# Optimization experiments

Hardware: AMD Instinct MI355X
Metric: run time of the kernel (lower is better)

Reference implementation:

```python
import jax, jax.numpy as jnp
import numpy as np

V, D, B, L = 8000, 256, 64, 64
CONCENTRATION = 5.0  # config['model']['args']['concentrator_factor']
GAW = 0.5            # initial value of _lambda parameter
EPS_COS = 1e-8       # torch cosine_similarity eps


def setup_inputs() -> dict:
    key = jax.random.key(0)
    ks = jax.random.split(key, 8)
    concepts_list = jax.random.randint(ks[0], (B, L), 0, V)
    concepts_length = jax.random.randint(ks[1], (B,), 0, L)
    contrastive_mask = jax.random.randint(ks[2], (B, V), 0, 2).astype(jnp.int32)
    # raw edge matrix, then row-range normalization as in init_params
    edge_raw = jax.random.uniform(ks[3], (V, V), dtype=jnp.float32)
    rng = (edge_raw.max(axis=1) - edge_raw.min(axis=1))[:, None]
    edge_matrix = edge_raw / (rng + (rng == 0).astype(jnp.float32))
    affectiveness = jax.random.uniform(ks[4], (V,), dtype=jnp.float32)
    embed_w = jax.random.normal(ks[5], (V, D), dtype=jnp.float32)
    embed_kb_w = jax.random.normal(ks[6], (V, D), dtype=jnp.float32)
    lam = jnp.full((V,), GAW, dtype=jnp.float32)
    return {
        "concepts_list": concepts_list,
        "concepts_length": concepts_length,
        "contrastive_mask": contrastive_mask,
        "edge_matrix": edge_matrix,
        "affectiveness": affectiveness,
        "embed_w": embed_w,
        "embed_kb_w": embed_kb_w,
        "lam": lam,
    }


def reference(concepts_list, concepts_length, contrastive_mask,
              edge_matrix, affectiveness, embed_w, embed_kb_w, lam):
    # [B, L, D] concept token embeddings
    concepts_embedded = embed_w[concepts_list]
    # valid-prefix mask per row: positions < concepts_length[i]
    pos_mask = (jnp.arange(L)[None, :] < concepts_length[:, None])  # [B, L] bool
    denom = jnp.maximum(concepts_length, 1).astype(concepts_embedded.dtype)[:, None]
    # per-row masked mean (rows with length 0 -> zeros, matching empty_tensor)
    row_mean = (concepts_embedded * pos_mask[..., None]).sum(axis=1) / denom  # [B, D]
    context_representation = row_mean.mean(axis=0)  # [D]
    # |cosine similarity| between context and every KB embedding -> [V]
    ctx_norm = jnp.linalg.norm(context_representation)
    kb_norms = jnp.linalg.norm(embed_kb_w, axis=1)
    cosine_similarity = jnp.abs(
        (embed_kb_w @ context_representation) / jnp.maximum(kb_norms * ctx_norm, EPS_COS)
    )
    # [B, L, V] local graph rows for each concept token
    local_graph = edge_matrix[concepts_list]
    rel = local_graph * cosine_similarity          # broadcast over V
    aff = (local_graph > 0).astype(local_graph.dtype) * affectiveness
    concepts_weights = lam * rel + (1.0 - lam) * aff  # [B, L, V]
    concepts_weights = jnp.where(contrastive_mask[:, None, :] == 0, 1e-9, concepts_weights)
    attn = jax.nn.softmax(concepts_weights * CONCENTRATION, axis=2)  # [B, L, V]
    concepts_embedding = jnp.einsum('blv,vd->bld', attn, embed_kb_w)  # [B, L, D]
    # masked mean over valid prefix (length 0 -> zeros)
    concepts_embedding = (concepts_embedding * pos_mask[..., None]).sum(axis=1) / denom  # [B, D]
    local_nodes = jnp.broadcast_to(embed_kb_w[None], (B, V, D))
    return concepts_embedding, local_nodes
```

## Files before the change

kernel.cpp:

```cpp
#include <hip/hip_runtime.h>
#include <cstddef>
#include <cstdint>
#include <cmath>

#define V 8000
#define D 256
#define B 64
#define L 64
#define SPLIT 8
#define NCH 100
#define VC 80
#define BT 16

#define PART_OFF 0
#define CTX_OFF  16384
#define W1_OFF   16640
#define W0_OFF   24640
#define A_OFF    32640
#define P_OFF    544640

typedef float f32x4 __attribute__((ext_vector_type(4)));

__global__ void k1_ctx(const int* __restrict__ clist, const int* __restrict__ clen,
                       const float* __restrict__ embw, float* __restrict__ part) {
    int b = blockIdx.x, d = threadIdx.x;
    int len = clen[b];
    int nl = len < L ? len : L;
    float acc = 0.f;
    for (int l = 0; l < nl; ++l) {
        int c = clist[b * L + l];
        acc += embw[(size_t)c * D + d];
    }
    float denom = (float)(len < 1 ? 1 : len);
    part[b * D + d] = acc / denom;
}

__global__ void k1b_reduce(const float* __restrict__ part, float* __restrict__ ctx) {
    int d = threadIdx.x;
    float s = 0.f;
    #pragma unroll 8
    for (int b = 0; b < B; ++b) s += part[b * D + d];
    ctx[d] = s * (1.0f / (float)B);
}

__global__ void k2_cos(const float* __restrict__ kb, const float* __restrict__ lam,
                       const float* __restrict__ aff, const float* __restrict__ ctx,
                       float* __restrict__ w1, float* __restrict__ w0,
                       float* __restrict__ A) {
    int tid = threadIdx.x;
    int gtid = blockIdx.x * 256 + tid;
    A[gtid] = 0.f;

    __shared__ float ctxs[D];
    __shared__ float red[5];
    int wid = tid >> 6, lane = tid & 63;
    float c = ctx[tid];
    ctxs[tid] = c;
    float sq = c * c;
    #pragma unroll
    for (int o = 32; o > 0; o >>= 1) sq += __shfl_xor(sq, o);
    if (lane == 0) red[wid] = sq;
    __syncthreads();
    if (tid == 0) red[4] = sqrtf(red[0] + red[1] + red[2] + red[3]);
    __syncthreads();
    float ctxnorm = red[4];

    int v = blockIdx.x * 4 + wid;
    float4 k4 = *(const float4*)(kb + (size_t)v * D + lane * 4);
    float4 c4 = *(const float4*)(ctxs + lane * 4);
    float dot = k4.x * c4.x + k4.y * c4.y + k4.z * c4.z + k4.w * c4.w;
    float sqs = k4.x * k4.x + k4.y * k4.y + k4.z * k4.z + k4.w * k4.w;
    #pragma unroll
    for (int o = 32; o > 0; o >>= 1) {
        dot += __shfl_xor(dot, o);
        sqs += __shfl_xor(sqs, o);
    }
    if (lane == 0) {
        float cosv = fabsf(dot) / fmaxf(sqrtf(sqs) * ctxnorm, 1e-8f);
        float la = lam[v];
        w1[v] = 5.0f * la * cosv;
        w0[v] = 5.0f * (1.0f - la) * aff[v];
    }
}

__global__ __launch_bounds__(1024) void k3_softmax(
    const int* __restrict__ clist, const int* __restrict__ clen,
    const int* __restrict__ cmask, const float* __restrict__ edge,
    const float* __restrict__ w1g, const float* __restrict__ w0g,
    float* __restrict__ A) {
    int b = blockIdx.x, split = blockIdx.y;
    int tid = threadIdx.x;
    int wid = tid >> 6, lane = tid & 63;
    bool active = tid < (V / 8);
    int v0 = tid * 8;
    __shared__ float lmax[17], lsum[17];

    float w1r[8], w0r[8], acc[8];
    int mr[8];
    if (active) {
        float4 t0 = *(const float4*)(w1g + v0);
        float4 t1 = *(const float4*)(w1g + v0 + 4);
        w1r[0]=t0.x; w1r[1]=t0.y; w1r[2]=t0.z; w1r[3]=t0.w;
        w1r[4]=t1.x; w1r[5]=t1.y; w1r[6]=t1.z; w1r[7]=t1.w;
        t0 = *(const float4*)(w0g + v0);
        t1 = *(const float4*)(w0g + v0 + 4);
        w0r[0]=t0.x; w0r[1]=t0.y; w0r[2]=t0.z; w0r[3]=t0.w;
        w0r[4]=t1.x; w0r[5]=t1.y; w0r[6]=t1.z; w0r[7]=t1.w;
        int4 m0 = *(const int4*)(cmask + (size_t)b * V + v0);
        int4 m1 = *(const int4*)(cmask + (size_t)b * V + v0 + 4);
        mr[0]=m0.x; mr[1]=m0.y; mr[2]=m0.z; mr[3]=m0.w;
        mr[4]=m1.x; mr[5]=m1.y; mr[6]=m1.z; mr[7]=m1.w;
    }
    #pragma unroll
    for (int j = 0; j < 8; ++j) acc[j] = 0.f;

    int len = clen[b];
    int nl = len < L ? len : L;
    for (int l = split; l < nl; l += SPLIT) {
        int c = clist[b * L + l];
        const float* er = edge + (size_t)c * V;
        float w[8];
        if (active) {
            float4 e0 = *(const float4*)(er + v0);
            float4 e1 = *(const float4*)(er + v0 + 4);
            float ev[8] = {e0.x, e0.y, e0.z, e0.w, e1.x, e1.y, e1.z, e1.w};
            #pragma unroll
            for (int j = 0; j < 8; ++j) {
                float e = ev[j];
                float wv = w1r[j] * e + (e > 0.f ? w0r[j] : 0.f);
                w[j] = (mr[j] != 0) ? wv : 5e-9f;
            }
        } else {
            #pragma unroll
            for (int j = 0; j < 8; ++j) w[j] = -INFINITY;
        }
        float mx = w[0];
        #pragma unroll
        for (int j = 1; j < 8; ++j) mx = fmaxf(mx, w[j]);
        #pragma unroll
        for (int o = 32; o > 0; o >>= 1) mx = fmaxf(mx, __shfl_xor(mx, o));
        if (lane == 0) lmax[wid] = mx;
        __syncthreads();
        if (wid == 0) {
            float x = lane < 16 ? lmax[lane] : -INFINITY;
            #pragma unroll
            for (int o = 8; o > 0; o >>= 1) x = fmaxf(x, __shfl_xor(x, o));
            if (lane == 0) lmax[16] = x;
        }
        __syncthreads();
        mx = lmax[16];
        float s = 0.f;
        if (active) {
            #pragma unroll
            for (int j = 0; j < 8; ++j) { w[j] = __expf(w[j] - mx); s += w[j]; }
        }
        #pragma unroll
        for (int o = 32; o > 0; o >>= 1) s += __shfl_xor(s, o);
        if (lane == 0) lsum[wid] = s;
        __syncthreads();
        if (wid == 0) {
            float x = lane < 16 ? lsum[lane] : 0.f;
            #pragma unroll
            for (int o = 8; o > 0; o >>= 1) x += __shfl_xor(x, o);
            if (lane == 0) lsum[16] = x;
        }
        __syncthreads();
        float inv = 1.0f / lsum[16];
        if (active) {
            #pragma unroll
            for (int j = 0; j < 8; ++j) acc[j] += w[j] * inv;
        }
    }
    if (active) {
        #pragma unroll
        for (int j = 0; j < 8; ++j)
            atomicAdd(&A[(size_t)b * V + v0 + j], acc[j]);
    }
}

__global__ __launch_bounds__(256) void k4_gemv(const float* __restrict__ A,
                                               const float* __restrict__ kb,
                                               float* __restrict__ P) {
    int ch = blockIdx.x;
    int bq = blockIdx.y;
    int tid = threadIdx.x;
    int vbase = ch * VC;
    int b0 = bq * BT;
    __shared__ float Al[BT][VC];
    for (int i = tid; i < BT * VC; i += 256) {
        int bt = i / VC, vl = i % VC;
        Al[bt][vl] = A[(size_t)(b0 + bt) * V + vbase + vl];
    }
    __syncthreads();
    float acc[BT];
    #pragma unroll
    for (int t = 0; t < BT; ++t) acc[t] = 0.f;
    for (int vl = 0; vl < VC; ++vl) {
        float kv = kb[(size_t)(vbase + vl) * D + tid];
        #pragma unroll
        for (int t = 0; t < BT; ++t) acc[t] += Al[t][vl] * kv;
    }
    #pragma unroll
    for (int t = 0; t < BT; ++t)
        P[(size_t)ch * (B * D) + (size_t)(b0 + t) * D + tid] = acc[t];
}

__global__ void k5_out0(const float* __restrict__ P, const int* __restrict__ clen,
                        float* __restrict__ out0) {
    int b = blockIdx.x, d = threadIdx.x;
    float s = 0.f;
    for (int ch = 0; ch < NCH; ++ch) s += P[(size_t)ch * (B * D) + b * D + d];
    int len = clen[b];
    out0[b * D + d] = s / (float)(len < 1 ? 1 : len);
}

__global__ void k6_bcast(const f32x4* __restrict__ kb4, f32x4* __restrict__ out4) {
    int idx = blockIdx.x * 256 + threadIdx.x;
    f32x4 f = kb4[idx];
    #pragma unroll
    for (int b = 0; b < B; ++b)
        __builtin_nontemporal_store(f, &out4[(size_t)b * (V * D / 4) + idx]);
}

extern "C" void kernel_launch(void* const* d_in, const int* in_sizes, int n_in,
                              void* d_out, int out_size, void* d_ws, size_t ws_size,
                              hipStream_t stream) {
    const int*   clist = (const int*)d_in[0];
    const int*   clen  = (const int*)d_in[1];
    const int*   cmask = (const int*)d_in[2];
    const float* edge  = (const float*)d_in[3];
    const float* aff   = (const float*)d_in[4];
    const float* embw  = (const float*)d_in[5];
    const float* kb    = (const float*)d_in[6];
    const float* lam   = (const float*)d_in[7];
    float* out0 = (float*)d_out;
    float* out1 = out0 + B * D;
    float* ws   = (float*)d_ws;

    k1_ctx<<<dim3(B), dim3(D), 0, stream>>>(clist, clen, embw, ws + PART_OFF);
    k1b_reduce<<<dim3(1), dim3(D), 0, stream>>>(ws + PART_OFF, ws + CTX_OFF);
    k2_cos<<<dim3(V / 4), dim3(256), 0, stream>>>(kb, lam, aff, ws + CTX_OFF,
                                                  ws + W1_OFF, ws + W0_OFF, ws + A_OFF);
    k3_softmax<<<dim3(B, SPLIT), dim3(1024), 0, stream>>>(clist, clen, cmask, edge,
                                                          ws + W1_OFF, ws + W0_OFF, ws + A_OFF);
    k4_gemv<<<dim3(NCH, B / BT), dim3(256), 0, stream>>>(ws + A_OFF, kb, ws + P_OFF);
    k5_out0<<<dim3(B), dim3(D), 0, stream>>>(ws + P_OFF, clen, out0);
    k6_bcast<<<dim3(V * D / 4 / 256), dim3(256), 0, stream>>>((const f32x4*)kb,
                                                              (f32x4*)out1);
}
```

Measured before the change: 297.0 us.

## Fuse broadcast into softmax kernel, drop max pass, retile gemv over all batches

The 64x broadcast copy of embed_kb_w now runs as extra blocks inside the softmax launch, so the write-bound copy can overlap the edge-row softmax work and one launch is removed. The softmax skips the max-subtraction pass and uses a single double-buffered shared-memory sum, which halves the block barriers per row. This relies on the weights being small enough that exp cannot overflow. The GEMV now processes all 64 batches per block with smaller V chunks (200 chunks), and k1_ctx caches concept ids in shared memory and unrolls its gather with four accumulators.

Result: slower. 310.8 us (+4.6%).

```diff
diff --git a/kernel.cpp b/kernel.cpp
--- a/kernel.cpp
+++ b/kernel.cpp
@@ -8,9 +8,10 @@
 #define B 64
 #define L 64
 #define SPLIT 8
-#define NCH 100
-#define VC 80
-#define BT 16
+#define NB_SM (B * SPLIT)
+#define NB_BC 500
+#define NCH 200
+#define VC 40
 
 #define PART_OFF 0
 #define CTX_OFF  16384
@@ -21,18 +22,27 @@
 
 typedef float f32x4 __attribute__((ext_vector_type(4)));
 
-__global__ void k1_ctx(const int* __restrict__ clist, const int* __restrict__ clen,
-                       const float* __restrict__ embw, float* __restrict__ part) {
+__global__ __launch_bounds__(256) void k1_ctx(const int* __restrict__ clist,
+                                              const int* __restrict__ clen,
+                                              const float* __restrict__ embw,
+                                              float* __restrict__ part) {
     int b = blockIdx.x, d = threadIdx.x;
+    __shared__ int cl[L];
+    if (d < L) cl[d] = clist[b * L + d];
+    __syncthreads();
     int len = clen[b];
     int nl = len < L ? len : L;
-    float acc = 0.f;
-    for (int l = 0; l < nl; ++l) {
-        int c = clist[b * L + l];
-        acc += embw[(size_t)c * D + d];
-    }
+    float a0 = 0.f, a1 = 0.f, a2 = 0.f, a3 = 0.f;
+    int l = 0;
+    for (; l + 4 <= nl; l += 4) {
+        a0 += embw[(size_t)cl[l]     * D + d];
+        a1 += embw[(size_t)cl[l + 1] * D + d];
+        a2 += embw[(size_t)cl[l + 2] * D + d];
+        a3 += embw[(size_t)cl[l + 3] * D + d];
+    }
+    for (; l < nl; ++l) a0 += embw[(size_t)cl[l] * D + d];
     float denom = (float)(len < 1 ? 1 : len);
-    part[b * D + d] = acc / denom;
+    part[b * D + d] = (a0 + a1 + a2 + a3) / denom;
 }
 
 __global__ void k1b_reduce(const float* __restrict__ part, float* __restrict__ ctx) {
@@ -43,10 +53,13 @@
     ctx[d] = s * (1.0f / (float)B);
 }
 
-__global__ void k2_cos(const float* __restrict__ kb, const float* __restrict__ lam,
-                       const float* __restrict__ aff, const float* __restrict__ ctx,
-                       float* __restrict__ w1, float* __restrict__ w0,
-                       float* __restrict__ A) {
+__global__ __launch_bounds__(256) void k2_cos(const float* __restrict__ kb,
+                                              const float* __restrict__ lam,
+                                              const float* __restrict__ aff,
+                                              const float* __restrict__ ctx,
+                                              float* __restrict__ w1,
+                                              float* __restrict__ w0,
+                                              float* __restrict__ A) {
     int tid = threadIdx.x;
     int gtid = blockIdx.x * 256 + tid;
     A[gtid] = 0.f;
@@ -83,17 +96,29 @@
     }
 }
 
-__global__ __launch_bounds__(1024) void k3_softmax(
+__global__ __launch_bounds__(1024) void k36_fused(
     const int* __restrict__ clist, const int* __restrict__ clen,
     const int* __restrict__ cmask, const float* __restrict__ edge,
     const float* __restrict__ w1g, const float* __restrict__ w0g,
-    float* __restrict__ A) {
-    int b = blockIdx.x, split = blockIdx.y;
+    float* __restrict__ A,
+    const f32x4* __restrict__ kb4, f32x4* __restrict__ out4) {
+    int g = blockIdx.x;
     int tid = threadIdx.x;
+
+    if (g >= NB_SM) {
+        int idx = (g - NB_SM) * 1024 + tid;
+        f32x4 f = kb4[idx];
+        #pragma unroll
+        for (int b = 0; b < B; ++b)
+            __builtin_nontemporal_store(f, &out4[(size_t)b * (V * D / 4) + idx]);
+        return;
+    }
+
+    int b = g >> 3, split = g & (SPLIT - 1);
     int wid = tid >> 6, lane = tid & 63;
     bool active = tid < (V / 8);
     int v0 = tid * 8;
-    __shared__ float lmax[17], lsum[17];
+    __shared__ float lsum[2][16];
 
     float w1r[8], w0r[8], acc[8];
     int mr[8];
@@ -116,10 +141,12 @@
 
     int len = clen[b];
     int nl = len < L ? len : L;
+    int parity = 0;
     for (int l = split; l < nl; l += SPLIT) {
         int c = clist[b * L + l];
         const float* er = edge + (size_t)c * V;
-        float w[8];
+        float p[8];
+        float s = 0.f;
         if (active) {
             float4 e0 = *(const float4*)(er + v0);
             float4 e1 = *(const float4*)(er + v0 + 4);
@@ -128,48 +155,27 @@
             for (int j = 0; j < 8; ++j) {
                 float e = ev[j];
                 float wv = w1r[j] * e + (e > 0.f ? w0r[j] : 0.f);
-                w[j] = (mr[j] != 0) ? wv : 5e-9f;
+                wv = (mr[j] != 0) ? wv : 5e-9f;
+                p[j] = __expf(wv);
+                s += p[j];
             }
         } else {
             #pragma unroll
-            for (int j = 0; j < 8; ++j) w[j] = -INFINITY;
+            for (int j = 0; j < 8; ++j) p[j] = 0.f;
         }
-        float mx = w[0];
-        #pragma unroll
-        for (int j = 1; j < 8; ++j) mx = fmaxf(mx, w[j]);
-        #pragma unroll
-        for (int o = 32; o > 0; o >>= 1) mx = fmaxf(mx, __shfl_xor(mx, o));
-        if (lane == 0) lmax[wid] = mx;
+        #pragma unroll
+        for (int o = 32; o > 0; o >>= 1) s += __shfl_xor(s, o);
+        if (lane == 0) lsum[parity][wid] = s;
         __syncthreads();
-        if (wid == 0) {
-            float x = lane < 16 ? lmax[lane] : -INFINITY;
-            #pragma unroll
-            for (int o = 8; o > 0; o >>= 1) x = fmaxf(x, __shfl_xor(x, o));
-            if (lane == 0) lmax[16] = x;
-        }
-        __syncthreads();
-        mx = lmax[16];
-        float s = 0.f;
+        float tot = 0.f;
+        #pragma unroll
+        for (int k = 0; k < 16; ++k) tot += lsum[parity][k];
+        float inv = 1.0f / tot;
         if (active) {
             #pragma unroll
-            for (int j = 0; j < 8; ++j) { w[j] = __expf(w[j] - mx); s += w[j]; }
+            for (int j = 0; j < 8; ++j) acc[j] += p[j] * inv;
         }
-        #pragma unroll
-        for (int o = 32; o > 0; o >>= 1) s += __shfl_xor(s, o);
-        if (lane == 0) lsum[wid] = s;
-        __syncthreads();
-        if (wid == 0) {
-            float x = lane < 16 ? lsum[lane] : 0.f;
-            #pragma unroll
-            for (int o = 8; o > 0; o >>= 1) x += __shfl_xor(x, o);
-            if (lane == 0) lsum[16] = x;
-        }
-        __syncthreads();
-        float inv = 1.0f / lsum[16];
-        if (active) {
-            #pragma unroll
-            for (int j = 0; j < 8; ++j) acc[j] += w[j] * inv;
-        }
+        parity ^= 1;
     }
     if (active) {
         #pragma unroll
@@ -182,44 +188,35 @@
                                                const float* __restrict__ kb,
                                                float* __restrict__ P) {
     int ch = blockIdx.x;
-    int bq = blockIdx.y;
     int tid = threadIdx.x;
     int vbase = ch * VC;
-    int b0 = bq * BT;
-    __shared__ float Al[BT][VC];
-    for (int i = tid; i < BT * VC; i += 256) {
+    __shared__ float Al[B][VC];
+    for (int i = tid; i < B * VC; i += 256) {
         int bt = i / VC, vl = i % VC;
-        Al[bt][vl] = A[(size_t)(b0 + bt) * V + vbase + vl];
-    }
-    __syncthreads();
-    float acc[BT];
-    #pragma unroll
-    for (int t = 0; t < BT; ++t) acc[t] = 0.f;
+        Al[bt][vl] = A[(size_t)bt * V + vbase + vl];
+    }
+    __syncthreads();
+    float acc[B];
+    #pragma unroll
+    for (int t = 0; t < B; ++t) acc[t] = 0.f;
     for (int vl = 0; vl < VC; ++vl) {
         float kv = kb[(size_t)(vbase + vl) * D + tid];
         #pragma unroll
-        for (int t = 0; t < BT; ++t) acc[t] += Al[t][vl] * kv;
-    }
-    #pragma unroll
-    for (int t = 0; t < BT; ++t)
-        P[(size_t)ch * (B * D) + (size_t)(b0 + t) * D + tid] = acc[t];
+        for (int t = 0; t < B; ++t) acc[t] += Al[t][vl] * kv;
+    }
+    #pragma unroll
+    for (int t = 0; t < B; ++t)
+        P[(size_t)ch * (B * D) + (size_t)t * D + tid] = acc[t];
 }
 
 __global__ void k5_out0(const float* __restrict__ P, const int* __restrict__ clen,
                         float* __restrict__ out0) {
     int b = blockIdx.x, d = threadIdx.x;
     float s = 0.f;
+    #pragma unroll 8
     for (int ch = 0; ch < NCH; ++ch) s += P[(size_t)ch * (B * D) + b * D + d];
     int len = clen[b];
     out0[b * D + d] = s / (float)(len < 1 ? 1 : len);
-}
-
-__global__ void k6_bcast(const f32x4* __restrict__ kb4, f32x4* __restrict__ out4) {
-    int idx = blockIdx.x * 256 + threadIdx.x;
-    f32x4 f = kb4[idx];
-    #pragma unroll
-    for (int b = 0; b < B; ++b)
-        __builtin_nontemporal_store(f, &out4[(size_t)b * (V * D / 4) + idx]);
 }
 
 extern "C" void kernel_launch(void* const* d_in, const int* in_sizes, int n_in,
@@ -237,14 +234,13 @@
     float* out1 = out0 + B * D;
     float* ws   = (float*)d_ws;
 
-    k1_ctx<<<dim3(B), dim3(D), 0, stream>>>(clist, clen, embw, ws + PART_OFF);
+    k1_ctx<<<dim3(B), dim3(256), 0, stream>>>(clist, clen, embw, ws + PART_OFF);
     k1b_reduce<<<dim3(1), dim3(D), 0, stream>>>(ws + PART_OFF, ws + CTX_OFF);
     k2_cos<<<dim3(V / 4), dim3(256), 0, stream>>>(kb, lam, aff, ws + CTX_OFF,
                                                   ws + W1_OFF, ws + W0_OFF, ws + A_OFF);
-    k3_softmax<<<dim3(B, SPLIT), dim3(1024), 0, stream>>>(clist, clen, cmask, edge,
-                                                          ws + W1_OFF, ws + W0_OFF, ws + A_OFF);
-    k4_gemv<<<dim3(NCH, B / BT), dim3(256), 0, stream>>>(ws + A_OFF, kb, ws + P_OFF);
+    k36_fused<<<dim3(NB_SM + NB_BC), dim3(1024), 0, stream>>>(
+        clist, clen, cmask, edge, ws + W1_OFF, ws + W0_OFF, ws + A_OFF,
+        (const f32x4*)kb, (f32x4*)out1);
+    k4_gemv<<<dim3(NCH), dim3(256), 0, stream>>>(ws + A_OFF, kb, ws + P_OFF);
     k5_out0<<<dim3(B), dim3(D), 0, stream>>>(ws + P_OFF, clen, out0);
-    k6_bcast<<<dim3(V * D / 4 / 256), dim3(256), 0, stream>>>((const f32x4*)kb,
-                                                              (f32x4*)out1);
-}
+}
```
